# Kernel tuning notes

Measured on AMD Instinct MI355X. Metric: run time of the kernel, lower is better.

The kernel has to match this reference:

```python
import jax, jax.numpy as jnp
import numpy as np

EMBED_DIM = 1024
NUM_HEADS = 16
EFF_HEADS = NUM_HEADS // 2
HEAD_DIM = EMBED_DIM // NUM_HEADS
LAMBDA_INIT = 0.8
B, N = 2, 2048


def setup_inputs() -> dict:
    key = jax.random.key(0)
    ks = jax.random.split(key, 14)
    s = 0.02
    return {
        "x": jax.random.normal(ks[0], (B, N, EMBED_DIM), dtype=jnp.float32),
        "Wq": jax.random.normal(ks[1], (EMBED_DIM, EMBED_DIM), dtype=jnp.float32) * s,
        "bq": jnp.zeros((EMBED_DIM,), dtype=jnp.float32),
        "Wk": jax.random.normal(ks[2], (EMBED_DIM, EMBED_DIM), dtype=jnp.float32) * s,
        "bk": jnp.zeros((EMBED_DIM,), dtype=jnp.float32),
        "Wv": jax.random.normal(ks[3], (EMBED_DIM, EMBED_DIM), dtype=jnp.float32) * s,
        "bv": jnp.zeros((EMBED_DIM,), dtype=jnp.float32),
        "Wp": jax.random.normal(ks[4], (EMBED_DIM, EMBED_DIM), dtype=jnp.float32) * s,
        "bp": jnp.zeros((EMBED_DIM,), dtype=jnp.float32),
        "lambda_q1": jax.random.normal(ks[5], (EFF_HEADS, 1, HEAD_DIM), dtype=jnp.float32) * s,
        "lambda_k1": jax.random.normal(ks[6], (EFF_HEADS, 1, HEAD_DIM), dtype=jnp.float32) * s,
        "lambda_q2": jax.random.normal(ks[7], (EFF_HEADS, 1, HEAD_DIM), dtype=jnp.float32) * s,
        "lambda_k2": jax.random.normal(ks[8], (EFF_HEADS, 1, HEAD_DIM), dtype=jnp.float32) * s,
    }


def reference(x, Wq, bq, Wk, bk, Wv, bv, Wp, bp,
              lambda_q1, lambda_k1, lambda_q2, lambda_k2):
    Bb, Nn, C = x.shape
    H, H2, hd = NUM_HEADS, EFF_HEADS, HEAD_DIM
    scale = hd ** (-0.5)

    # projections (torch Linear: y = x @ W.T + b), reshape to [B,H,N,hd]
    q = (x @ Wq.T + bq).reshape(Bb, Nn, H, hd).transpose(0, 2, 1, 3)
    k = (x @ Wk.T + bk).reshape(Bb, Nn, H, hd).transpose(0, 2, 1, 3)
    v = (x @ Wv.T + bv).reshape(Bb, Nn, H, hd).transpose(0, 2, 1, 3)

    q1, q2 = q[:, :H2], q[:, H2:]
    k1, k2 = k[:, :H2], k[:, H2:]
    v1, v2 = v[:, :H2], v[:, H2:]

    # scalar lambda: per-head dot products, clamped exp, differenced, averaged
    l1 = jnp.exp(jnp.minimum((lambda_q1 * lambda_k1).sum((-1, -2)), 5.0))  # [H2]
    l2 = jnp.exp(jnp.minimum((lambda_q2 * lambda_k2).sum((-1, -2)), 5.0))
    lv = (l1 - l2 + LAMBDA_INIT).mean()

    a1 = jax.nn.softmax(jnp.einsum('bhnd,bhmd->bhnm', q1, k1) * scale, axis=-1)
    x1 = jnp.einsum('bhnm,bhmd->bhnd', a1, v1).transpose(0, 2, 1, 3).reshape(Bb, Nn, C // 2)
    a2 = jax.nn.softmax(jnp.einsum('bhnd,bhmd->bhnm', q2, k2) * scale, axis=-1)
    x2 = jnp.einsum('bhnm,bhmd->bhnd', a2, v2).transpose(0, 2, 1, 3).reshape(Bb, Nn, C // 2)

    out = jnp.concatenate([x1 - lv * x2, x2], axis=-1) @ Wp.T + bp
    return out
```

## Files before the change

kernel.cpp:

```cpp
#include <hip/hip_runtime.h>

typedef __bf16 bf16;
typedef __bf16 bf16x8 __attribute__((ext_vector_type(8)));
typedef __bf16 bf16x4 __attribute__((ext_vector_type(4)));
typedef float  f32x16 __attribute__((ext_vector_type(16)));
typedef unsigned int uint;
typedef unsigned int uintx4 __attribute__((ext_vector_type(4)));

#define QSCALE (0.125f * 1.44269504088896340736f)

__device__ __forceinline__ void g2l16(const void* g, void* l) {
  __builtin_amdgcn_global_load_lds(
      (const __attribute__((address_space(1))) void*)g,
      (__attribute__((address_space(3))) void*)l, 16, 0, 0);
}

__device__ __forceinline__ f32x16 mfma16(bf16x8 a, bf16x8 b, f32x16 c) {
  return __builtin_amdgcn_mfma_f32_32x32x16_bf16(a, b, c, 0, 0, 0);
}

__device__ __forceinline__ uint pack_bf16(float a, float b) {
  unsigned short lo = __builtin_bit_cast(unsigned short, (bf16)a);
  unsigned short hi = __builtin_bit_cast(unsigned short, (bf16)b);
  return (uint)lo | ((uint)hi << 16);
}

__global__ void cast5_kernel(const float* __restrict__ x,
                             const float* __restrict__ wq, const float* __restrict__ wk,
                             const float* __restrict__ wv, const float* __restrict__ wp,
                             bf16* __restrict__ xb, bf16* __restrict__ wqkv,
                             bf16* __restrict__ wpb) {
  int seg = blockIdx.y;
  long i = (long)(blockIdx.x * 256 + threadIdx.x) * 8;
  const float* s; bf16* d; long n;
  if (seg == 0)      { s = x;  d = xb;  n = 4194304; }
  else if (seg == 1) { s = wq; d = wqkv;            n = 1048576; }
  else if (seg == 2) { s = wk; d = wqkv + 1048576;  n = 1048576; }
  else if (seg == 3) { s = wv; d = wqkv + 2097152;  n = 1048576; }
  else               { s = wp; d = wpb;             n = 1048576; }
  if (i >= n) return;
  float4 f0 = *(const float4*)(s + i);
  float4 f1 = *(const float4*)(s + i + 4);
  bf16x8 o;
  o[0] = (bf16)f0.x; o[1] = (bf16)f0.y; o[2] = (bf16)f0.z; o[3] = (bf16)f0.w;
  o[4] = (bf16)f1.x; o[5] = (bf16)f1.y; o[6] = (bf16)f1.z; o[7] = (bf16)f1.w;
  *(bf16x8*)(d + i) = o;
}

__global__ void lv_kernel(const float* __restrict__ lq1, const float* __restrict__ lk1,
                          const float* __restrict__ lq2, const float* __restrict__ lk2,
                          float* __restrict__ lvp) {
  int t = threadIdx.x;
  float accum = 0.f;
  for (int hh = 0; hh < 8; ++hh) {
    float v1 = lq1[hh*64 + t] * lk1[hh*64 + t];
    float v2 = lq2[hh*64 + t] * lk2[hh*64 + t];
    for (int off = 32; off; off >>= 1) {
      v1 += __shfl_xor(v1, off);
      v2 += __shfl_xor(v2, off);
    }
    accum += expf(fminf(v1, 5.f)) - expf(fminf(v2, 5.f));
  }
  if (t == 0) *lvp = accum / 8.f + 0.8f;
}

__global__ __launch_bounds__(256, 2) void gemm_qkv_kernel(
    const bf16* __restrict__ A, const bf16* __restrict__ B,
    const float* __restrict__ bias0, const float* __restrict__ bias1,
    const float* __restrict__ bias2,
    bf16* __restrict__ O0, bf16* __restrict__ O1, bf16* __restrict__ O2) {
  __shared__ __align__(16) char smem[32 * 1024];
  const int tid = threadIdx.x;
  const int w = tid >> 6, L = tid & 63;
  const int l31 = L & 31, h5 = L >> 5;
  const int m0 = blockIdx.x * 128;
  const int n0g = blockIdx.y * 128;
  const int by = n0g >> 10;
  const bf16* Bp = B + (long)by * 1048576;
  const float* biasp = (by == 0) ? bias0 : ((by == 1) ? bias1 : bias2);
  const int nloc = n0g & 1023;

  f32x16 acc[2][2];
  for (int i = 0; i < 2; ++i) for (int j = 0; j < 2; ++j)
    for (int r = 0; r < 16; ++r) acc[i][j][r] = 0.f;

  const int srow = L >> 1, spar = L & 1;
  const int wm = w >> 1, wn = w & 1;
  const int fs = (l31 * 2 + h5) * 16;

  for (int k0 = 0; k0 < 1024; k0 += 64) {
    for (int i = 0; i < 8; ++i) {
      int r = w * 8 + i;
      int rr = r & 15;
      int rowblk = rr >> 2, kst = rr & 3;
      int row = rowblk * 32 + srow;
      int kk = k0 + (kst * 2 + spar) * 8;
      const bf16* gsrc = (r < 16) ? (A + (long)(m0 + row) * 1024 + kk)
                                  : (Bp + (long)(nloc + row) * 1024 + kk);
      g2l16(gsrc, smem + r * 1024);
    }
    __syncthreads();
    for (int kst = 0; kst < 4; ++kst) {
      bf16x8 a0 = *(const bf16x8*)(smem + (((wm * 2 + 0) * 4 + kst) * 1024) + fs);
      bf16x8 a1 = *(const bf16x8*)(smem + (((wm * 2 + 1) * 4 + kst) * 1024) + fs);
      bf16x8 b0 = *(const bf16x8*)(smem + 16384 + (((wn * 2 + 0) * 4 + kst) * 1024) + fs);
      bf16x8 b1 = *(const bf16x8*)(smem + 16384 + (((wn * 2 + 1) * 4 + kst) * 1024) + fs);
      acc[0][0] = mfma16(a0, b0, acc[0][0]);
      acc[0][1] = mfma16(a0, b1, acc[0][1]);
      acc[1][0] = mfma16(a1, b0, acc[1][0]);
      acc[1][1] = mfma16(a1, b1, acc[1][1]);
    }
    __syncthreads();
  }

  if (by == 2) {
    int b = m0 >> 11;
    int nbase = (m0 & 2047);
    for (int mi = 0; mi < 2; ++mi) for (int ni = 0; ni < 2; ++ni) {
      int col = nloc + wn * 64 + ni * 32 + l31;
      int hh = col >> 6, d = col & 63;
      float bias_v = biasp[col];
      long rowbase = ((long)(b * 16 + hh) * 64 + d) * 2048
                   + nbase + wm * 64 + mi * 32 + 4 * h5;
      for (int g = 0; g < 4; ++g) {
        bf16x4 pk;
        for (int r = 0; r < 4; ++r) pk[r] = (bf16)(acc[mi][ni][g * 4 + r] + bias_v);
        *(bf16x4*)(O2 + rowbase + 8 * g) = pk;
      }
    }
  } else {
    bf16* dst = (by == 0) ? O0 : O1;
    float scale = (by == 0) ? QSCALE : 1.0f;
    for (int mi = 0; mi < 2; ++mi) for (int ni = 0; ni < 2; ++ni) {
      int col = nloc + wn * 64 + ni * 32 + l31;
      float bias_v = biasp[col];
      int row_base = m0 + wm * 64 + mi * 32 + 4 * h5;
      for (int reg = 0; reg < 16; ++reg) {
        int rowoff = (reg & 3) + 8 * (reg >> 2);
        float v = (acc[mi][ni][reg] + bias_v) * scale;
        dst[(long)(row_base + rowoff) * 1024 + col] = (bf16)v;
      }
    }
  }
}

__global__ __launch_bounds__(256, 2) void gemm_proj_kernel(
    const bf16* __restrict__ A, const bf16* __restrict__ B,
    const float* __restrict__ bias, float* __restrict__ Of) {
  __shared__ __align__(16) char smem[24 * 1024];
  const int tid = threadIdx.x;
  const int w = tid >> 6, L = tid & 63;
  const int l31 = L & 31, h5 = L >> 5;
  const int m0 = blockIdx.x * 64;
  const int nloc = blockIdx.y * 128;

  f32x16 acc[2];
  for (int i = 0; i < 2; ++i)
    for (int r = 0; r < 16; ++r) acc[i][r] = 0.f;

  const int srow = L >> 1, spar = L & 1;
  const int fs = (l31 * 2 + h5) * 16;

  for (int k0 = 0; k0 < 1024; k0 += 64) {
    for (int i = 0; i < 6; ++i) {
      int r = w * 6 + i;
      const bf16* gsrc;
      if (r < 8) {
        int rowblk = r >> 2, kst = r & 3;
        gsrc = A + (long)(m0 + rowblk * 32 + srow) * 1024 + k0 + (kst * 2 + spar) * 8;
      } else {
        int rr = r - 8;
        int rowblk = rr >> 2, kst = rr & 3;
        gsrc = B + (long)(nloc + rowblk * 32 + srow) * 1024 + k0 + (kst * 2 + spar) * 8;
      }
      g2l16(gsrc, smem + r * 1024);
    }
    __syncthreads();
    for (int kst = 0; kst < 4; ++kst) {
      bf16x8 a0 = *(const bf16x8*)(smem + ((0 * 4 + kst) * 1024) + fs);
      bf16x8 a1 = *(const bf16x8*)(smem + ((1 * 4 + kst) * 1024) + fs);
      bf16x8 bb = *(const bf16x8*)(smem + 8192 + ((w * 4 + kst) * 1024) + fs);
      acc[0] = mfma16(a0, bb, acc[0]);
      acc[1] = mfma16(a1, bb, acc[1]);
    }
    __syncthreads();
  }

  for (int mi = 0; mi < 2; ++mi) {
    int col = nloc + w * 32 + l31;
    float bias_v = bias[col];
    int row_base = m0 + mi * 32 + 4 * h5;
    for (int reg = 0; reg < 16; ++reg) {
      int rowoff = (reg & 3) + 8 * (reg >> 2);
      Of[(long)(row_base + rowoff) * 1024 + col] = acc[mi][reg] + bias_v;
    }
  }
}

__global__ __launch_bounds__(512, 4) void attn_kernel(
    const bf16* __restrict__ Qb, const bf16* __restrict__ Kb,
    const bf16* __restrict__ Vt, bf16* __restrict__ Ob) {
  __shared__ __align__(16) char smem[34816];
  const int tid = threadIdx.x, w = tid >> 6, L = tid & 63;
  const int half = w >> 2, pair = w & 3;
  const int bh = blockIdx.x, qt = blockIdx.y;
  const int b = bh >> 4, h = bh & 15;
  const int q0 = qt * 128 + pair * 32;
  const int l31 = L & 31, h5 = L >> 5;
  const int srow = L >> 1, spar = L & 1;
  const int fs = (l31 * 2 + h5) * 16;
  char* kbase = smem + half * 16384;

  bf16x8 qf[4];
  for (int kst = 0; kst < 4; ++kst)
    qf[kst] = *(const bf16x8*)(Qb + (long)(b * 2048 + q0 + l31) * 1024 + h * 64
                               + kst * 16 + h5 * 8);

  f32x16 o[2];
  for (int i = 0; i < 2; ++i)
    for (int r = 0; r < 16; ++r) o[i][r] = 0.f;
  float lsum = 0.f;

  const bf16* Kbh = Kb + (long)b * 2048 * 1024 + h * 64 + (long)half * 1024 * 1024;
  const bf16* Vth = Vt + (long)bh * 64 * 2048 + half * 1024;

  for (int t = 0; t < 16; ++t) {
    int n0 = t * 64;
    for (int i = 0; i < 4; ++i) {
      int r = pair * 4 + i;
      if (r < 8) {
        int nkb = r >> 2, kst = r & 3;
        const bf16* g = Kbh + (long)(n0 + nkb * 32 + srow) * 1024 + (kst * 2 + spar) * 8;
        g2l16(g, kbase + r * 1024);
      } else {
        int rr = r - 8, db = rr >> 2, kst = rr & 3;
        const bf16* g = Vth + (long)(db * 32 + srow) * 2048 + n0 + (kst * 2 + spar) * 8;
        g2l16(g, kbase + 8192 + rr * 1024);
      }
    }
    __syncthreads();

    f32x16 s[2];
    for (int i = 0; i < 2; ++i)
      for (int r = 0; r < 16; ++r) s[i][r] = 0.f;
    for (int kst = 0; kst < 4; ++kst) {
      bf16x8 k0f = *(const bf16x8*)(kbase + ((0 * 4 + kst) * 1024) + fs);
      bf16x8 k1f = *(const bf16x8*)(kbase + ((4 + kst) * 1024) + fs);
      s[0] = mfma16(k0f, qf[kst], s[0]);
      s[1] = mfma16(k1f, qf[kst], s[1]);
    }

    for (int nki = 0; nki < 2; ++nki)
      for (int r = 0; r < 16; ++r) {
        float p = __builtin_amdgcn_exp2f(s[nki][r]);
        s[nki][r] = p;
        lsum += p;
      }

    for (int kst = 0; kst < 4; ++kst) {
      bf16x8 v0 = *(const bf16x8*)(kbase + 8192 + ((0 * 4 + kst) * 1024) + fs);
      bf16x8 v1 = *(const bf16x8*)(kbase + 8192 + ((4 + kst) * 1024) + fs);
      int nki = kst >> 1;
      int rbase = (kst & 1) * 8;
      uint p0a = pack_bf16(s[nki][rbase + 0], s[nki][rbase + 1]);
      uint p0b = pack_bf16(s[nki][rbase + 2], s[nki][rbase + 3]);
      uint p1a = pack_bf16(s[nki][rbase + 4], s[nki][rbase + 5]);
      uint p1b = pack_bf16(s[nki][rbase + 6], s[nki][rbase + 7]);
      uint t0 = h5 ? p0a : p1a;
      uint t1 = h5 ? p0b : p1b;
      uint r0 = (uint)__shfl_xor((int)t0, 32);
      uint r1 = (uint)__shfl_xor((int)t1, 32);
      uintx4 uv;
      uv.x = h5 ? r0 : p0a;
      uv.y = h5 ? r1 : p0b;
      uv.z = h5 ? p1a : r0;
      uv.w = h5 ? p1b : r1;
      bf16x8 pf = __builtin_bit_cast(bf16x8, uv);
      o[0] = mfma16(v0, pf, o[0]);
      o[1] = mfma16(v1, pf, o[1]);
    }
    __syncthreads();
  }

  float lcol = lsum + __shfl_xor(lsum, 32);
  if (half) {
    float* dstO = (float*)smem + pair * 2112;
    for (int di = 0; di < 2; ++di)
      for (int r = 0; r < 16; ++r) dstO[L * 33 + di * 16 + r] = o[di][r];
    if (h5 == 0) ((float*)(smem + 33792))[pair * 32 + l31] = lcol;
  }
  __syncthreads();
  float linv = 0.f;
  if (!half) {
    float* srcO = (float*)smem + pair * 2112;
    for (int di = 0; di < 2; ++di)
      for (int r = 0; r < 16; ++r) o[di][r] += srcO[L * 33 + di * 16 + r];
    float lother = ((float*)(smem + 33792))[pair * 32 + l31];
    linv = 1.f / (lcol + lother);
  }
  __syncthreads();
  if (!half) {
    char* ot = smem + pair * 4352;
    for (int di = 0; di < 2; ++di)
      for (int g = 0; g < 4; ++g) {
        bf16x4 pk;
        for (int r = 0; r < 4; ++r)
          pk[r] = (bf16)(o[di][g * 4 + r] * linv);
        int d0 = di * 32 + g * 8 + h5 * 4;
        *(bf16x4*)(ot + (l31 * 68 + d0) * 2) = pk;
      }
    for (int i = 0; i < 4; ++i) {
      int qloc = (L >> 3) + i * 8;
      int cc = L & 7;
      bf16x8 vv = *(const bf16x8*)(ot + (qloc * 68 + cc * 8) * 2);
      *(bf16x8*)(Ob + (long)(b * 2048 + q0 + qloc) * 1024 + h * 64 + cc * 8) = vv;
    }
  }
}

__global__ void combine_kernel(bf16* __restrict__ Ob, const float* __restrict__ lvp) {
  float lv = *lvp;
  int idx = blockIdx.x * 256 + threadIdx.x;
  int row = idx >> 6;
  int j = (idx & 63) * 8;
  bf16x8 o1 = *(const bf16x8*)(Ob + (long)row * 1024 + j);
  bf16x8 o2 = *(const bf16x8*)(Ob + (long)row * 1024 + 512 + j);
  bf16x8 c1;
  for (int e = 0; e < 8; ++e) c1[e] = (bf16)((float)o1[e] - lv * (float)o2[e]);
  *(bf16x8*)(Ob + (long)row * 1024 + j) = c1;
}

extern "C" void kernel_launch(void* const* d_in, const int* in_sizes, int n_in,
                              void* d_out, int out_size, void* d_ws, size_t ws_size,
                              hipStream_t stream) {
  const float* x   = (const float*)d_in[0];
  const float* Wq  = (const float*)d_in[1];
  const float* bq  = (const float*)d_in[2];
  const float* Wk  = (const float*)d_in[3];
  const float* bk  = (const float*)d_in[4];
  const float* Wv  = (const float*)d_in[5];
  const float* bv  = (const float*)d_in[6];
  const float* Wp  = (const float*)d_in[7];
  const float* bp  = (const float*)d_in[8];
  const float* lq1 = (const float*)d_in[9];
  const float* lk1 = (const float*)d_in[10];
  const float* lq2 = (const float*)d_in[11];
  const float* lk2 = (const float*)d_in[12];
  float* out = (float*)d_out;

  char* ws = (char*)d_ws;
  float* lvp = (float*)ws;
  bf16* xb   = (bf16*)(ws + 1024);
  bf16* Wqkv = xb + (long)4096 * 1024;
  bf16* Wpb  = Wqkv + (long)3 * 1024 * 1024;
  bf16* Vt   = Wpb + (long)1024 * 1024;
  bf16* Ob   = Vt + (long)4096 * 1024;
  bf16* Qb = (bf16*)d_out;
  bf16* Kb = Qb + (long)4096 * 1024;

  cast5_kernel<<<dim3(2048, 5), 256, 0, stream>>>(x, Wq, Wk, Wv, Wp, xb, Wqkv, Wpb);
  lv_kernel<<<1, 64, 0, stream>>>(lq1, lk1, lq2, lk2, lvp);
  gemm_qkv_kernel<<<dim3(32, 24), 256, 0, stream>>>(
      xb, Wqkv, bq, bk, bv, Qb, Kb, Vt);
  attn_kernel<<<dim3(32, 16), 512, 0, stream>>>(Qb, Kb, Vt, Ob);
  combine_kernel<<<1024, 256, 0, stream>>>(Ob, lvp);
  gemm_proj_kernel<<<dim3(64, 8), 256, 0, stream>>>(Ob, Wpb, bp, out);
}
```

Baseline: 210.0 us.

## Fold lambda combine into projection weights and double attention KV tile

The x1 - lv*x2 combine is folded algebraically into the bf16 cast of Wp: the second-half columns become Wp2 - lv*Wp1, so the separate combine pass over the attention output goes away. lv_kernel now launches before the cast. Separately, the attention kernel processes 128 keys per iteration instead of 64, doubling LDS to 64KB and lowering the launch-bounds occupancy hint. Fewer barriers and tile loads are traded for lower occupancy, and folding lv into the weights changes where bf16 rounding happens.

```diff
diff --git a/kernel.cpp b/kernel.cpp
--- a/kernel.cpp
+++ b/kernel.cpp
@@ -25,9 +25,27 @@
   return (uint)lo | ((uint)hi << 16);
 }
 
+__global__ void lv_kernel(const float* __restrict__ lq1, const float* __restrict__ lk1,
+                          const float* __restrict__ lq2, const float* __restrict__ lk2,
+                          float* __restrict__ lvp) {
+  int t = threadIdx.x;
+  float accum = 0.f;
+  for (int hh = 0; hh < 8; ++hh) {
+    float v1 = lq1[hh*64 + t] * lk1[hh*64 + t];
+    float v2 = lq2[hh*64 + t] * lk2[hh*64 + t];
+    for (int off = 32; off; off >>= 1) {
+      v1 += __shfl_xor(v1, off);
+      v2 += __shfl_xor(v2, off);
+    }
+    accum += expf(fminf(v1, 5.f)) - expf(fminf(v2, 5.f));
+  }
+  if (t == 0) *lvp = accum / 8.f + 0.8f;
+}
+
 __global__ void cast5_kernel(const float* __restrict__ x,
                              const float* __restrict__ wq, const float* __restrict__ wk,
                              const float* __restrict__ wv, const float* __restrict__ wp,
+                             const float* __restrict__ lvp,
                              bf16* __restrict__ xb, bf16* __restrict__ wqkv,
                              bf16* __restrict__ wpb) {
   int seg = blockIdx.y;
@@ -41,27 +59,17 @@
   if (i >= n) return;
   float4 f0 = *(const float4*)(s + i);
   float4 f1 = *(const float4*)(s + i + 4);
+  if (seg == 4 && (i & 1023) >= 512) {
+    float lv = *lvp;
+    float4 g0 = *(const float4*)(s + i - 512);
+    float4 g1 = *(const float4*)(s + i - 508);
+    f0.x -= lv * g0.x; f0.y -= lv * g0.y; f0.z -= lv * g0.z; f0.w -= lv * g0.w;
+    f1.x -= lv * g1.x; f1.y -= lv * g1.y; f1.z -= lv * g1.z; f1.w -= lv * g1.w;
+  }
   bf16x8 o;
   o[0] = (bf16)f0.x; o[1] = (bf16)f0.y; o[2] = (bf16)f0.z; o[3] = (bf16)f0.w;
   o[4] = (bf16)f1.x; o[5] = (bf16)f1.y; o[6] = (bf16)f1.z; o[7] = (bf16)f1.w;
   *(bf16x8*)(d + i) = o;
-}
-
-__global__ void lv_kernel(const float* __restrict__ lq1, const float* __restrict__ lk1,
-                          const float* __restrict__ lq2, const float* __restrict__ lk2,
-                          float* __restrict__ lvp) {
-  int t = threadIdx.x;
-  float accum = 0.f;
-  for (int hh = 0; hh < 8; ++hh) {
-    float v1 = lq1[hh*64 + t] * lk1[hh*64 + t];
-    float v2 = lq2[hh*64 + t] * lk2[hh*64 + t];
-    for (int off = 32; off; off >>= 1) {
-      v1 += __shfl_xor(v1, off);
-      v2 += __shfl_xor(v2, off);
-    }
-    accum += expf(fminf(v1, 5.f)) - expf(fminf(v2, 5.f));
-  }
-  if (t == 0) *lvp = accum / 8.f + 0.8f;
 }
 
 __global__ __launch_bounds__(256, 2) void gemm_qkv_kernel(
@@ -197,10 +205,10 @@
   }
 }
 
-__global__ __launch_bounds__(512, 4) void attn_kernel(
+__global__ __launch_bounds__(512, 2) void attn_kernel(
     const bf16* __restrict__ Qb, const bf16* __restrict__ Kb,
     const bf16* __restrict__ Vt, bf16* __restrict__ Ob) {
-  __shared__ __align__(16) char smem[34816];
+  __shared__ __align__(16) char smem[65536];
   const int tid = threadIdx.x, w = tid >> 6, L = tid & 63;
   const int half = w >> 2, pair = w & 3;
   const int bh = blockIdx.x, qt = blockIdx.y;
@@ -209,7 +217,7 @@
   const int l31 = L & 31, h5 = L >> 5;
   const int srow = L >> 1, spar = L & 1;
   const int fs = (l31 * 2 + h5) * 16;
-  char* kbase = smem + half * 16384;
+  char* kbase = smem + half * 32768;
 
   bf16x8 qf[4];
   for (int kst = 0; kst < 4; ++kst)
@@ -224,48 +232,48 @@
   const bf16* Kbh = Kb + (long)b * 2048 * 1024 + h * 64 + (long)half * 1024 * 1024;
   const bf16* Vth = Vt + (long)bh * 64 * 2048 + half * 1024;
 
-  for (int t = 0; t < 16; ++t) {
-    int n0 = t * 64;
-    for (int i = 0; i < 4; ++i) {
-      int r = pair * 4 + i;
-      if (r < 8) {
+  for (int t = 0; t < 8; ++t) {
+    int n0 = t * 128;
+    for (int i = 0; i < 8; ++i) {
+      int r = pair * 8 + i;
+      if (r < 16) {
         int nkb = r >> 2, kst = r & 3;
         const bf16* g = Kbh + (long)(n0 + nkb * 32 + srow) * 1024 + (kst * 2 + spar) * 8;
         g2l16(g, kbase + r * 1024);
       } else {
-        int rr = r - 8, db = rr >> 2, kst = rr & 3;
-        const bf16* g = Vth + (long)(db * 32 + srow) * 2048 + n0 + (kst * 2 + spar) * 8;
-        g2l16(g, kbase + 8192 + rr * 1024);
-      }
-    }
-    __syncthreads();
-
-    f32x16 s[2];
-    for (int i = 0; i < 2; ++i)
-      for (int r = 0; r < 16; ++r) s[i][r] = 0.f;
+        int rr = r - 16, di = rr >> 3, kc = rr & 7;
+        const bf16* g = Vth + (long)(di * 32 + srow) * 2048 + n0 + (kc * 2 + spar) * 8;
+        g2l16(g, kbase + 16384 + rr * 1024);
+      }
+    }
+    __syncthreads();
+
+    f32x16 s[4];
+    for (int kb = 0; kb < 4; ++kb)
+      for (int r = 0; r < 16; ++r) s[kb][r] = 0.f;
     for (int kst = 0; kst < 4; ++kst) {
-      bf16x8 k0f = *(const bf16x8*)(kbase + ((0 * 4 + kst) * 1024) + fs);
-      bf16x8 k1f = *(const bf16x8*)(kbase + ((4 + kst) * 1024) + fs);
-      s[0] = mfma16(k0f, qf[kst], s[0]);
-      s[1] = mfma16(k1f, qf[kst], s[1]);
-    }
-
-    for (int nki = 0; nki < 2; ++nki)
+      for (int kb = 0; kb < 4; ++kb) {
+        bf16x8 kf = *(const bf16x8*)(kbase + ((kb * 4 + kst) * 1024) + fs);
+        s[kb] = mfma16(kf, qf[kst], s[kb]);
+      }
+    }
+
+    for (int kb = 0; kb < 4; ++kb)
       for (int r = 0; r < 16; ++r) {
-        float p = __builtin_amdgcn_exp2f(s[nki][r]);
-        s[nki][r] = p;
+        float p = __builtin_amdgcn_exp2f(s[kb][r]);
+        s[kb][r] = p;
         lsum += p;
       }
 
-    for (int kst = 0; kst < 4; ++kst) {
-      bf16x8 v0 = *(const bf16x8*)(kbase + 8192 + ((0 * 4 + kst) * 1024) + fs);
-      bf16x8 v1 = *(const bf16x8*)(kbase + 8192 + ((4 + kst) * 1024) + fs);
-      int nki = kst >> 1;
-      int rbase = (kst & 1) * 8;
-      uint p0a = pack_bf16(s[nki][rbase + 0], s[nki][rbase + 1]);
-      uint p0b = pack_bf16(s[nki][rbase + 2], s[nki][rbase + 3]);
-      uint p1a = pack_bf16(s[nki][rbase + 4], s[nki][rbase + 5]);
-      uint p1b = pack_bf16(s[nki][rbase + 6], s[nki][rbase + 7]);
+    for (int kc = 0; kc < 8; ++kc) {
+      bf16x8 v0 = *(const bf16x8*)(kbase + 16384 + (kc * 1024) + fs);
+      bf16x8 v1 = *(const bf16x8*)(kbase + 16384 + ((8 + kc) * 1024) + fs);
+      int kb = kc >> 1;
+      int rbase = (kc & 1) * 8;
+      uint p0a = pack_bf16(s[kb][rbase + 0], s[kb][rbase + 1]);
+      uint p0b = pack_bf16(s[kb][rbase + 2], s[kb][rbase + 3]);
+      uint p1a = pack_bf16(s[kb][rbase + 4], s[kb][rbase + 5]);
+      uint p1b = pack_bf16(s[kb][rbase + 6], s[kb][rbase + 7]);
       uint t0 = h5 ? p0a : p1a;
       uint t1 = h5 ? p0b : p1b;
       uint r0 = (uint)__shfl_xor((int)t0, 32);
@@ -316,18 +324,6 @@
       *(bf16x8*)(Ob + (long)(b * 2048 + q0 + qloc) * 1024 + h * 64 + cc * 8) = vv;
     }
   }
-}
-
-__global__ void combine_kernel(bf16* __restrict__ Ob, const float* __restrict__ lvp) {
-  float lv = *lvp;
-  int idx = blockIdx.x * 256 + threadIdx.x;
-  int row = idx >> 6;
-  int j = (idx & 63) * 8;
-  bf16x8 o1 = *(const bf16x8*)(Ob + (long)row * 1024 + j);
-  bf16x8 o2 = *(const bf16x8*)(Ob + (long)row * 1024 + 512 + j);
-  bf16x8 c1;
-  for (int e = 0; e < 8; ++e) c1[e] = (bf16)((float)o1[e] - lv * (float)o2[e]);
-  *(bf16x8*)(Ob + (long)row * 1024 + j) = c1;
 }
 
 extern "C" void kernel_launch(void* const* d_in, const int* in_sizes, int n_in,
@@ -358,11 +354,10 @@
   bf16* Qb = (bf16*)d_out;
   bf16* Kb = Qb + (long)4096 * 1024;
 
-  cast5_kernel<<<dim3(2048, 5), 256, 0, stream>>>(x, Wq, Wk, Wv, Wp, xb, Wqkv, Wpb);
   lv_kernel<<<1, 64, 0, stream>>>(lq1, lk1, lq2, lk2, lvp);
+  cast5_kernel<<<dim3(2048, 5), 256, 0, stream>>>(x, Wq, Wk, Wv, Wp, lvp, xb, Wqkv, Wpb);
   gemm_qkv_kernel<<<dim3(32, 24), 256, 0, stream>>>(
       xb, Wqkv, bq, bk, bv, Qb, Kb, Vt);
   attn_kernel<<<dim3(32, 16), 512, 0, stream>>>(Qb, Kb, Vt, Ob);
-  combine_kernel<<<1024, 256, 0, stream>>>(Ob, lvp);
   gemm_proj_kernel<<<dim3(64, 8), 256, 0, stream>>>(Ob, Wpb, bp, out);
 }
```

Measured after the change: 224.6 us. 7.0% more time.

## Fold lambda combine into projection weights and route P through LDS

Applied to the files above, without the earlier changes.

The lambda scalar is now computed inside the cast kernel, and the x1 - lv*x2 combination is folded algebraically into the projection weight (Wp's second-half columns become Wp2 - lv*Wp1). This removes the lv kernel and the combine kernel, along with their launches and an extra pass over Ob. Separately, the attention kernel no longer rearranges P fragments with cross-lane shuffles; it writes P to a per-wave LDS scratch row and reads it back. That raises LDS use per block from about 34 KB to 51 KB, which may reduce occupancy.

```diff
diff --git a/kernel.cpp b/kernel.cpp
--- a/kernel.cpp
+++ b/kernel.cpp
@@ -5,7 +5,7 @@
 typedef __bf16 bf16x4 __attribute__((ext_vector_type(4)));
 typedef float  f32x16 __attribute__((ext_vector_type(16)));
 typedef unsigned int uint;
-typedef unsigned int uintx4 __attribute__((ext_vector_type(4)));
+typedef unsigned int uintx2 __attribute__((ext_vector_type(2)));
 
 #define QSCALE (0.125f * 1.44269504088896340736f)
 
@@ -28,6 +28,8 @@
 __global__ void cast5_kernel(const float* __restrict__ x,
                              const float* __restrict__ wq, const float* __restrict__ wk,
                              const float* __restrict__ wv, const float* __restrict__ wp,
+                             const float* __restrict__ lq1, const float* __restrict__ lk1,
+                             const float* __restrict__ lq2, const float* __restrict__ lk2,
                              bf16* __restrict__ xb, bf16* __restrict__ wqkv,
                              bf16* __restrict__ wpb) {
   int seg = blockIdx.y;
@@ -41,27 +43,28 @@
   if (i >= n) return;
   float4 f0 = *(const float4*)(s + i);
   float4 f1 = *(const float4*)(s + i + 4);
+  if (seg == 4 && (i & 1023) >= 512) {
+    int t = threadIdx.x & 63;
+    float accum = 0.f;
+    for (int hh = 0; hh < 8; ++hh) {
+      float v1 = lq1[hh*64 + t] * lk1[hh*64 + t];
+      float v2 = lq2[hh*64 + t] * lk2[hh*64 + t];
+      for (int off = 32; off; off >>= 1) {
+        v1 += __shfl_xor(v1, off);
+        v2 += __shfl_xor(v2, off);
+      }
+      accum += expf(fminf(v1, 5.f)) - expf(fminf(v2, 5.f));
+    }
+    float lv = accum / 8.f + 0.8f;
+    float4 g0 = *(const float4*)(s + i - 512);
+    float4 g1 = *(const float4*)(s + i - 508);
+    f0.x -= lv * g0.x; f0.y -= lv * g0.y; f0.z -= lv * g0.z; f0.w -= lv * g0.w;
+    f1.x -= lv * g1.x; f1.y -= lv * g1.y; f1.z -= lv * g1.z; f1.w -= lv * g1.w;
+  }
   bf16x8 o;
   o[0] = (bf16)f0.x; o[1] = (bf16)f0.y; o[2] = (bf16)f0.z; o[3] = (bf16)f0.w;
   o[4] = (bf16)f1.x; o[5] = (bf16)f1.y; o[6] = (bf16)f1.z; o[7] = (bf16)f1.w;
   *(bf16x8*)(d + i) = o;
-}
-
-__global__ void lv_kernel(const float* __restrict__ lq1, const float* __restrict__ lk1,
-                          const float* __restrict__ lq2, const float* __restrict__ lk2,
-                          float* __restrict__ lvp) {
-  int t = threadIdx.x;
-  float accum = 0.f;
-  for (int hh = 0; hh < 8; ++hh) {
-    float v1 = lq1[hh*64 + t] * lk1[hh*64 + t];
-    float v2 = lq2[hh*64 + t] * lk2[hh*64 + t];
-    for (int off = 32; off; off >>= 1) {
-      v1 += __shfl_xor(v1, off);
-      v2 += __shfl_xor(v2, off);
-    }
-    accum += expf(fminf(v1, 5.f)) - expf(fminf(v2, 5.f));
-  }
-  if (t == 0) *lvp = accum / 8.f + 0.8f;
 }
 
 __global__ __launch_bounds__(256, 2) void gemm_qkv_kernel(
@@ -200,7 +203,7 @@
 __global__ __launch_bounds__(512, 4) void attn_kernel(
     const bf16* __restrict__ Qb, const bf16* __restrict__ Kb,
     const bf16* __restrict__ Vt, bf16* __restrict__ Ob) {
-  __shared__ __align__(16) char smem[34816];
+  __shared__ __align__(16) char smem[51200];
   const int tid = threadIdx.x, w = tid >> 6, L = tid & 63;
   const int half = w >> 2, pair = w & 3;
   const int bh = blockIdx.x, qt = blockIdx.y;
@@ -210,6 +213,7 @@
   const int srow = L >> 1, spar = L & 1;
   const int fs = (l31 * 2 + h5) * 16;
   char* kbase = smem + half * 16384;
+  char* prow = smem + 32768 + w * 2304 + l31 * 72;
 
   bf16x8 qf[4];
   for (int kst = 0; kst < 4; ++kst)
@@ -257,27 +261,21 @@
         lsum += p;
       }
 
-    for (int kst = 0; kst < 4; ++kst) {
-      bf16x8 v0 = *(const bf16x8*)(kbase + 8192 + ((0 * 4 + kst) * 1024) + fs);
-      bf16x8 v1 = *(const bf16x8*)(kbase + 8192 + ((4 + kst) * 1024) + fs);
-      int nki = kst >> 1;
-      int rbase = (kst & 1) * 8;
-      uint p0a = pack_bf16(s[nki][rbase + 0], s[nki][rbase + 1]);
-      uint p0b = pack_bf16(s[nki][rbase + 2], s[nki][rbase + 3]);
-      uint p1a = pack_bf16(s[nki][rbase + 4], s[nki][rbase + 5]);
-      uint p1b = pack_bf16(s[nki][rbase + 6], s[nki][rbase + 7]);
-      uint t0 = h5 ? p0a : p1a;
-      uint t1 = h5 ? p0b : p1b;
-      uint r0 = (uint)__shfl_xor((int)t0, 32);
-      uint r1 = (uint)__shfl_xor((int)t1, 32);
-      uintx4 uv;
-      uv.x = h5 ? r0 : p0a;
-      uv.y = h5 ? r1 : p0b;
-      uv.z = h5 ? p1a : r0;
-      uv.w = h5 ? p1b : r1;
-      bf16x8 pf = __builtin_bit_cast(bf16x8, uv);
-      o[0] = mfma16(v0, pf, o[0]);
-      o[1] = mfma16(v1, pf, o[1]);
+    for (int nki = 0; nki < 2; ++nki) {
+      for (int g = 0; g < 4; ++g) {
+        uintx2 pk;
+        pk.x = pack_bf16(s[nki][g * 4 + 0], s[nki][g * 4 + 1]);
+        pk.y = pack_bf16(s[nki][g * 4 + 2], s[nki][g * 4 + 3]);
+        *(uintx2*)(prow + (g * 8 + 4 * h5) * 2) = pk;
+      }
+      for (int c = 0; c < 2; ++c) {
+        int kst = nki * 2 + c;
+        bf16x8 pf = *(const bf16x8*)(prow + (c * 16 + h5 * 8) * 2);
+        bf16x8 v0 = *(const bf16x8*)(kbase + 8192 + ((0 * 4 + kst) * 1024) + fs);
+        bf16x8 v1 = *(const bf16x8*)(kbase + 8192 + ((4 + kst) * 1024) + fs);
+        o[0] = mfma16(v0, pf, o[0]);
+        o[1] = mfma16(v1, pf, o[1]);
+      }
     }
     __syncthreads();
   }
@@ -316,18 +314,6 @@
       *(bf16x8*)(Ob + (long)(b * 2048 + q0 + qloc) * 1024 + h * 64 + cc * 8) = vv;
     }
   }
-}
-
-__global__ void combine_kernel(bf16* __restrict__ Ob, const float* __restrict__ lvp) {
-  float lv = *lvp;
-  int idx = blockIdx.x * 256 + threadIdx.x;
-  int row = idx >> 6;
-  int j = (idx & 63) * 8;
-  bf16x8 o1 = *(const bf16x8*)(Ob + (long)row * 1024 + j);
-  bf16x8 o2 = *(const bf16x8*)(Ob + (long)row * 1024 + 512 + j);
-  bf16x8 c1;
-  for (int e = 0; e < 8; ++e) c1[e] = (bf16)((float)o1[e] - lv * (float)o2[e]);
-  *(bf16x8*)(Ob + (long)row * 1024 + j) = c1;
 }
 
 extern "C" void kernel_launch(void* const* d_in, const int* in_sizes, int n_in,
@@ -349,7 +335,6 @@
   float* out = (float*)d_out;
 
   char* ws = (char*)d_ws;
-  float* lvp = (float*)ws;
   bf16* xb   = (bf16*)(ws + 1024);
   bf16* Wqkv = xb + (long)4096 * 1024;
   bf16* Wpb  = Wqkv + (long)3 * 1024 * 1024;
@@ -358,11 +343,10 @@
   bf16* Qb = (bf16*)d_out;
   bf16* Kb = Qb + (long)4096 * 1024;
 
-  cast5_kernel<<<dim3(2048, 5), 256, 0, stream>>>(x, Wq, Wk, Wv, Wp, xb, Wqkv, Wpb);
-  lv_kernel<<<1, 64, 0, stream>>>(lq1, lk1, lq2, lk2, lvp);
+  cast5_kernel<<<dim3(2048, 5), 256, 0, stream>>>(
+      x, Wq, Wk, Wv, Wp, lq1, lk1, lq2, lk2, xb, Wqkv, Wpb);
   gemm_qkv_kernel<<<dim3(32, 24), 256, 0, stream>>>(
       xb, Wqkv, bq, bk, bv, Qb, Kb, Vt);
   attn_kernel<<<dim3(32, 16), 512, 0, stream>>>(Qb, Kb, Vt, Ob);
-  combine_kernel<<<1024, 256, 0, stream>>>(Ob, lvp);
   gemm_proj_kernel<<<dim3(64, 8), 256, 0, stream>>>(Ob, Wpb, bp, out);
 }
```

New measurement: 222.6 us. 1.06x slower.
